# Kernel optimization log

Measured on AMD Instinct MI355X. Metric: run time of the kernel, lower is better.

Reference implementation:

```python
import jax, jax.numpy as jnp
import numpy as np

H = 1024      # hidden_size
NH = 16       # num_attention_heads
DH = H // NH  # head_dim
EPS_LN = 1e-5


def _ln(x, g, b):
    m = x.mean(-1, keepdims=True)
    v = ((x - m) ** 2).mean(-1, keepdims=True)
    return (x - m) * jax.lax.rsqrt(v + EPS_LN) * g + b


def _gelu(x):
    return jax.nn.gelu(x, approximate=False)


def _split_heads(x, B, S):
    return x.reshape(B, S, NH, DH).transpose(0, 2, 1, 3)  # [B,NH,S,DH]


def setup_inputs() -> dict:
    key = jax.random.key(0)
    ks = jax.random.split(key, 16)
    std = 0.02
    d = {
        'hidden_states': jax.random.normal(ks[0], (4, 1024, H), jnp.float32),
        'wq': jax.random.normal(ks[1], (H, H), jnp.float32) * std,
        'wk': jax.random.normal(ks[2], (H, H), jnp.float32) * std,
        'wv': jax.random.normal(ks[3], (H, H), jnp.float32) * std,
        'wo': jax.random.normal(ks[4], (H, H), jnp.float32) * std,
        'mha_in_w': jax.random.normal(ks[5], (3 * H, H), jnp.float32) * std,   # nn.MultiheadAttention in_proj (no bias)
        'mha_out_w': jax.random.normal(ks[6], (H, H), jnp.float32) * std,
        'wt': jax.random.normal(ks[7], (NH, H), jnp.float32) * std,            # W_t
        'ttm_ln_g': jnp.ones((NH,), jnp.float32),
        'ttm_ln_b': jnp.zeros((NH,), jnp.float32),
        'thp_w': jax.random.normal(ks[8], (H, NH), jnp.float32) * std,         # temp_hidden_proj Linear(NH->H)
        'thp_b': jnp.zeros((H,), jnp.float32),
        'thp_ln_g': jnp.ones((H,), jnp.float32),
        'thp_ln_b': jnp.zeros((H,), jnp.float32),
        'tn_w1': jax.random.normal(ks[9], (H, 2 * H), jnp.float32) * std,      # temp_net Linear(2H->H)
        'tn_b1': jnp.zeros((H,), jnp.float32),
        'tn_ln_g': jnp.ones((H,), jnp.float32),
        'tn_ln_b': jnp.zeros((H,), jnp.float32),
        'tn_w2': jax.random.normal(ks[10], (1, H), jnp.float32) * std,         # temp_net Linear(H->1)
        'tn_b2': jnp.zeros((1,), jnp.float32),
    }
    return d


def reference(hidden_states, wq, wk, wv, wo, mha_in_w, mha_out_w, wt,
              ttm_ln_g, ttm_ln_b, thp_w, thp_b, thp_ln_g, thp_ln_b,
              tn_w1, tn_b1, tn_ln_g, tn_ln_b, tn_w2, tn_b2):
    x = hidden_states
    B, S, _ = x.shape
    scale = DH ** -0.5

    # ---- compute_ttm: T(x) = sigmoid(LN(W_t @ MHA(x,x,x))) (eval mode, step<100 branch) ----
    qkv = jnp.einsum('bsh,oh->bso', x, mha_in_w)  # [B,S,3H]
    mq, mk, mv = jnp.split(qkv, 3, axis=-1)
    mq, mk, mv = (_split_heads(t, B, S) for t in (mq, mk, mv))
    mprob = jax.nn.softmax(jnp.einsum('bhqd,bhkd->bhqk', mq, mk) * scale, axis=-1)
    mctx = jnp.einsum('bhqk,bhkd->bhqd', mprob, mv).transpose(0, 2, 1, 3).reshape(B, S, H)
    ttm_out = jnp.einsum('bsh,oh->bso', mctx, mha_out_w)
    temp = jax.nn.sigmoid(_ln(jnp.einsum('bsh,nh->bsn', ttm_out, wt), ttm_ln_g, ttm_ln_b))
    T0 = 1.0 + 0.1 * (temp - 0.5)  # [B,S,NH]

    # ---- compute_gsot ----
    T_base = jax.nn.sigmoid(_gelu(_ln(jnp.einsum('bsn,hn->bsh', T0, thp_w) + thp_b, thp_ln_g, thp_ln_b)))  # [B,S,H]
    temps = [T_base[:, :, 0:1]]
    for _ in range(2):
        comb = jnp.concatenate([x, T_base], axis=-1)  # [B,S,2H]
        h = _gelu(_ln(jnp.einsum('bsc,hc->bsh', comb, tn_w1) + tn_b1, tn_ln_g, tn_ln_b))
        Ti = jax.nn.sigmoid(jax.nn.sigmoid(jnp.einsum('bsh,oh->bso', h, tn_w2) + tn_b2))  # double sigmoid, [B,S,1]
        temps.append(Ti)
        T_base = jnp.broadcast_to(Ti, (B, S, H))
    scale_temps = jnp.stack(temps, axis=1)  # [B,3,S,1]

    # ---- temperature weights: normalized over the broadcast [B,NH,S,S] tensor ----
    tw = scale_temps.mean(axis=1)  # [B,S,1]
    Nt = B * NH * S * S            # expanded element count (torch .std() is unbiased over it)
    mu = tw.mean()
    var_b = ((tw - mu) ** 2).mean()
    std_u = jnp.sqrt(var_b * (Nt / (Nt - 1)))
    eps = jnp.finfo(tw.dtype).eps
    twn = 1.0 + (tw - mu) / (std_u + eps)  # [B,S,1], per-query scalar

    # ---- main attention ----
    q = _split_heads(jnp.einsum('bsh,oh->bso', x, wq), B, S)
    k = _split_heads(jnp.einsum('bsh,oh->bso', x, wk), B, S)
    v = _split_heads(jnp.einsum('bsh,oh->bso', x, wv), B, S)
    scores = jnp.einsum('bhqd,bhkd->bhqk', q, k) * scale
    scores = scores * twn[:, None, :, :]  # broadcast over heads and keys
    probs = jax.nn.softmax(scores, axis=-1)
    ctx = jnp.einsum('bhqk,bhkd->bhqd', probs, v).transpose(0, 2, 1, 3).reshape(B, S, H)
    context = jnp.einsum('bsh,oh->bso', ctx, wo)
    return (context, scale_temps)
```

## Files before the change

### kernel.cpp

```cpp
#include <hip/hip_runtime.h>
#include <hip/hip_bf16.h>

#define DEV __device__ __forceinline__

typedef short bf16x8 __attribute__((ext_vector_type(8)));
typedef short bf16x4 __attribute__((ext_vector_type(4)));
typedef float f32x4 __attribute__((ext_vector_type(4)));

static constexpr int B_  = 4;
static constexpr int S_  = 1024;
static constexpr int H_  = 1024;
static constexpr int NH_ = 16;
static constexpr int DH_ = 64;
static constexpr int BS_ = B_ * S_;
static constexpr int H6_ = 6 * H_;

DEV void gld16(const void* g, void* l) {
  __builtin_amdgcn_global_load_lds(
      (__attribute__((address_space(1))) void*)(unsigned long long)g,
      (__attribute__((address_space(3))) void*)(unsigned)(unsigned long long)l,
      16, 0, 0);
}

DEV f32x4 pv_mfma(bf16x4 a, bf16x4 b, f32x4 c) {
#if __has_builtin(__builtin_amdgcn_mfma_f32_16x16x16bf16_1k)
  return __builtin_amdgcn_mfma_f32_16x16x16bf16_1k(a, b, c, 0, 0, 0);
#else
  asm volatile("v_mfma_f32_16x16x16_bf16 %0, %1, %2, %0" : "+v"(c) : "v"(a), "v"(b));
  return c;
#endif
}

DEV float wred_sum(float v) {
#pragma unroll
  for (int o = 32; o; o >>= 1) v += __shfl_xor(v, o);
  return v;
}
DEV float bred_sum(float v, float* sh) {
  v = wred_sum(v);
  const int tid = threadIdx.x;
  if ((tid & 63) == 0) sh[tid >> 6] = v;
  __syncthreads();
  v = sh[0] + sh[1] + sh[2] + sh[3];
  __syncthreads();
  return v;
}
DEV float geluf(float x) { return 0.5f * x * (1.f + erff(x * 0.70710678118654752f)); }

struct CastSeg { const float* src; unsigned short* dst; int n; };
struct PrepArgs {
  CastSeg s[7];
  const float* wt; const float* wout; float* weff;
  const float* w1; float* rsum;
};
__global__ __launch_bounds__(256) void prep_k(PrepArgs a) {
  const int y = blockIdx.y, tid = threadIdx.x;
  if (y < 7) {
    const CastSeg g = a.s[y];
    int i = (blockIdx.x * 256 + tid) * 4;
    if (i >= g.n) return;
    float4 v = *(const float4*)(g.src + i);
    __hip_bfloat16 o0 = __float2bfloat16(v.x), o1 = __float2bfloat16(v.y);
    __hip_bfloat16 o2 = __float2bfloat16(v.z), o3 = __float2bfloat16(v.w);
    ushort4 o;
    o.x = *(unsigned short*)&o0; o.y = *(unsigned short*)&o1;
    o.z = *(unsigned short*)&o2; o.w = *(unsigned short*)&o3;
    *(ushort4*)(g.dst + i) = o;
  } else if (y == 7) {
    if (blockIdx.x >= 256) return;
    const int h = (blockIdx.x & 15) * 64 + (tid & 63), ng = tid >> 6;
    const int o0 = (blockIdx.x >> 4) * 64;
    float acc[4] = {0.f, 0.f, 0.f, 0.f};
#pragma unroll 8
    for (int o = o0; o < o0 + 64; o++) {
      float wv = a.wout[(size_t)o * H_ + h];
#pragma unroll
      for (int i = 0; i < 4; i++) acc[i] += a.wt[(size_t)(ng * 4 + i) * H_ + o] * wv;
    }
#pragma unroll
    for (int i = 0; i < 4; i++) atomicAdd(&a.weff[(size_t)(ng * 4 + i) * H_ + h], acc[i]);
  } else {
    if (blockIdx.x >= 256) return;
    const int row = blockIdx.x * 4 + (tid >> 6), lane = tid & 63;
    float s = 0.f;
#pragma unroll
    for (int j = 0; j < 16; j++) s += a.w1[(size_t)row * 2048 + 1024 + lane + j * 64];
    s = wred_sum(s);
    if (lane == 0) a.rsum[row] = s;
  }
}

__global__ __launch_bounds__(256) void gemm_qkv_k(
    const __hip_bfloat16* __restrict__ Ap, const __hip_bfloat16* __restrict__ Wp,
    __hip_bfloat16* __restrict__ Cp, __hip_bfloat16* __restrict__ vt2) {
  constexpr int BK = 32;
  __shared__ __align__(16) short smem[8448];
  short* sA = smem;
  short* sB = smem + 4096;
  short* sT = smem;
  const int tid = threadIdx.x;
  const int wave = tid >> 6, lane = tid & 63;
  const int wm = wave >> 1, wn = wave & 1;
  const int lr = lane & 15, kq = lane >> 4;
  const int bx = blockIdx.x, by = blockIdx.y;
  const short* Ab = (const short*)Ap + (long long)by * 128 * H_;
  const short* Wb = (const short*)Wp + (long long)bx * 128 * H_;

  f32x4 acc[4][4];
#pragma unroll
  for (int i = 0; i < 4; i++)
#pragma unroll
    for (int j = 0; j < 4; j++) acc[i][j] = f32x4{0.f, 0.f, 0.f, 0.f};

  for (int k0 = 0; k0 < H_; k0 += BK) {
#pragma unroll
    for (int r = 0; r < 2; r++) {
      int idx = r * 256 + tid;
      gld16(Ab + (long long)(idx >> 2) * H_ + k0 + (idx & 3) * 8, sA + (size_t)idx * 8);
    }
#pragma unroll
    for (int r = 0; r < 2; r++) {
      int idx = r * 256 + tid;
      gld16(Wb + (long long)(idx >> 2) * H_ + k0 + (idx & 3) * 8, sB + (size_t)idx * 8);
    }
    __syncthreads();
    bf16x8 af[4], bfr[4];
#pragma unroll
    for (int i = 0; i < 4; i++)
      af[i] = *(const bf16x8*)(sA + (wm * 64 + i * 16 + lr) * BK + kq * 8);
#pragma unroll
    for (int j = 0; j < 4; j++)
      bfr[j] = *(const bf16x8*)(sB + (wn * 64 + j * 16 + lr) * BK + kq * 8);
#pragma unroll
    for (int i = 0; i < 4; i++)
#pragma unroll
      for (int j = 0; j < 4; j++)
        acc[i][j] = __builtin_amdgcn_mfma_f32_16x16x32_bf16(af[i], bfr[j], acc[i][j], 0, 0, 0);
    __syncthreads();
  }

  const bool isV = (bx >= 16 && bx < 24) || (bx >= 40);
  if (!isV) {
    const long long row0 = (long long)by * 128 + wm * 64 + kq * 4;
    const long long col0 = (long long)bx * 128 + wn * 64 + lr;
#pragma unroll
    for (int i = 0; i < 4; i++)
#pragma unroll
      for (int j = 0; j < 4; j++)
#pragma unroll
        for (int r = 0; r < 4; r++)
          Cp[(row0 + i * 16 + r) * H6_ + col0 + j * 16] = __float2bfloat16(acc[i][j][r]);
  } else {
    const int sel = bx >= 40;
    const int h0 = (bx - (sel ? 40 : 16)) * 2;
    const int b = by >> 3, s0 = (by & 7) * 128;
#pragma unroll
    for (int hh = 0; hh < 2; hh++) {
      __syncthreads();
      if (wn == hh) {
#pragma unroll
        for (int i = 0; i < 4; i++)
#pragma unroll
          for (int j = 0; j < 4; j++)
#pragma unroll
            for (int r = 0; r < 4; r++) {
              __hip_bfloat16 v = __float2bfloat16(acc[i][j][r]);
              sT[(j * 16 + lr) * 132 + wm * 64 + i * 16 + kq * 4 + r] = *(short*)&v;
            }
      }
      __syncthreads();
      const int bh2 = sel * 64 + b * 16 + h0 + hh;
      short* dst = (short*)vt2 + (size_t)bh2 * DH_ * S_ + s0;
#pragma unroll
      for (int c = 0; c < 8; c++) {
        int flat = c * 256 + tid;
        int d = flat >> 5, s4 = (flat & 31) * 4;
        *(short4*)(dst + (size_t)d * S_ + s4) = *(short4*)(sT + d * 132 + s4);
      }
    }
  }
}

template <int MT, int NT, int WR, int WC, bool MID>
__global__ __launch_bounds__(256) void gemm_bt(
    const __hip_bfloat16* __restrict__ Ap, const __hip_bfloat16* __restrict__ Wp,
    float* __restrict__ Cp, int K, int lda, int ldw, int ldc,
    const __hip_bfloat16* __restrict__ Ap2, float* __restrict__ Cmid, int kmid) {
  constexpr int BM = WR * MT * 16;
  constexpr int BN = WC * NT * 16;
  constexpr int BK = 32;
  __shared__ __align__(16) short sA[BM * BK];
  __shared__ __align__(16) short sB[BN * BK];
  const int tid = threadIdx.x;
  const int wave = tid >> 6, lane = tid & 63;
  const int wm = wave / WC, wn = wave % WC;
  const int lr = lane & 15, kq = lane >> 4;
  const short* Ab = (const short*)Ap + (long long)blockIdx.y * BM * lda;
  const short* Ab2 = MID ? (const short*)Ap2 + (long long)blockIdx.y * BM * lda : nullptr;
  const short* Wb = (const short*)Wp + (long long)blockIdx.x * BN * ldw;
  const long long row0 = (long long)blockIdx.y * BM + wm * MT * 16 + kq * 4;
  const long long col0 = (long long)blockIdx.x * BN + wn * NT * 16 + lr;

  f32x4 acc[MT][NT];
#pragma unroll
  for (int i = 0; i < MT; i++)
#pragma unroll
    for (int j = 0; j < NT; j++) acc[i][j] = f32x4{0.f, 0.f, 0.f, 0.f};

  for (int k0 = 0; k0 < K; k0 += BK) {
    const short* Asrc;
    int ka;
    if (MID && k0 >= kmid) { Asrc = Ab2; ka = k0 - kmid; }
    else { Asrc = Ab; ka = k0; }
#pragma unroll
    for (int r = 0; r < BM / 64; r++) {
      int idx = r * 256 + tid;
      gld16(Asrc + (long long)(idx >> 2) * lda + ka + (idx & 3) * 8, sA + (size_t)idx * 8);
    }
#pragma unroll
    for (int r = 0; r < BN / 64; r++) {
      int idx = r * 256 + tid;
      gld16(Wb + (long long)(idx >> 2) * ldw + k0 + (idx & 3) * 8, sB + (size_t)idx * 8);
    }
    __syncthreads();
    bf16x8 af[MT], bfr[NT];
#pragma unroll
    for (int i = 0; i < MT; i++)
      af[i] = *(const bf16x8*)(sA + (wm * MT * 16 + i * 16 + lr) * BK + kq * 8);
#pragma unroll
    for (int j = 0; j < NT; j++)
      bfr[j] = *(const bf16x8*)(sB + (wn * NT * 16 + j * 16 + lr) * BK + kq * 8);
#pragma unroll
    for (int i = 0; i < MT; i++)
#pragma unroll
      for (int j = 0; j < NT; j++)
        acc[i][j] = __builtin_amdgcn_mfma_f32_16x16x32_bf16(af[i], bfr[j], acc[i][j], 0, 0, 0);
    if constexpr (MID) {
      if (k0 + BK == kmid) {
#pragma unroll
        for (int i = 0; i < MT; i++)
#pragma unroll
          for (int j = 0; j < NT; j++)
#pragma unroll
            for (int r = 0; r < 4; r++)
              Cmid[(row0 + i * 16 + r) * ldc + col0 + j * 16] = acc[i][j][r];
      }
    }
    __syncthreads();
  }
#pragma unroll
  for (int i = 0; i < MT; i++)
#pragma unroll
    for (int j = 0; j < NT; j++)
#pragma unroll
      for (int r = 0; r < 4; r++)
        Cp[(row0 + i * 16 + r) * ldc + col0 + j * 16] = acc[i][j][r];
}

template <bool TTM>
__global__ __launch_bounds__(256) void flash_k(
    const __hip_bfloat16* __restrict__ qkvB,
    const __hip_bfloat16* __restrict__ vt,
    const float* __restrict__ twn,
    __hip_bfloat16* __restrict__ ctx,
    float scale, int ldq) {
  __shared__ __align__(16) short sK[2][128 * 64];
  __shared__ __align__(16) short sVT[2][64 * 128];
  const int bh = blockIdx.x, b = bh >> 4, h = bh & 15;
  const int qb = blockIdx.y;
  const int tid = threadIdx.x, lane = tid & 63, wid = tid >> 6;
  const int lr = lane & 15, quad = lane >> 4;
  const short* qg = (const short*)qkvB + ((size_t)(b * S_) + qb * 128) * ldq + h * 64;
  const short* kg = (const short*)qkvB + (size_t)b * S_ * ldq + H_ + h * 64;
  const short* vg = (const short*)vt + (size_t)bh * DH_ * S_;

  auto stage = [&](int kt, int buf) {
#pragma unroll
    for (int i = 0; i < 4; i++) {
      int idx = i * 256 + tid;
      int row = idx >> 3, cp = idx & 7;
      int c = cp ^ (row & 7);
      gld16(kg + (size_t)(kt * 128 + row) * ldq + c * 8, &sK[buf][(size_t)idx * 8]);
    }
#pragma unroll
    for (int i = 0; i < 4; i++) {
      int idx = i * 256 + tid;
      int row = idx >> 4, cp = idx & 15;
      int c = cp ^ (row & 15);
      gld16(vg + (size_t)row * S_ + kt * 128 + c * 8, &sVT[buf][(size_t)idx * 8]);
    }
  };

  bf16x8 bq[2][2];
#pragma unroll
  for (int nt = 0; nt < 2; nt++)
#pragma unroll
    for (int kk = 0; kk < 2; kk++)
      bq[nt][kk] =
          *(const bf16x8*)(qg + (size_t)(wid * 32 + nt * 16 + lr) * ldq + kk * 32 + quad * 8);

  float fs[2];
#pragma unroll
  for (int nt = 0; nt < 2; nt++) {
    int q = qb * 128 + wid * 32 + nt * 16 + lr;
    fs[nt] = TTM ? scale : scale * twn[b * S_ + q];
  }
  f32x4 O[2][4];
#pragma unroll
  for (int nt = 0; nt < 2; nt++)
#pragma unroll
    for (int dt = 0; dt < 4; dt++) O[nt][dt] = f32x4{0.f, 0.f, 0.f, 0.f};
  float lrow[2] = {0.f, 0.f};

  stage(0, 0);
  __syncthreads();

  for (int kt = 0; kt < 8; kt++) {
    const int cur = kt & 1;
    if (kt < 7) stage(kt + 1, cur ^ 1);
    const short* sKc = sK[cur];
    const short* sVc = sVT[cur];

    f32x4 Sa[8][2];
#pragma unroll
    for (int mt = 0; mt < 8; mt++)
#pragma unroll
      for (int nt = 0; nt < 2; nt++) Sa[mt][nt] = f32x4{0.f, 0.f, 0.f, 0.f};
#pragma unroll
    for (int mt = 0; mt < 8; mt++)
#pragma unroll
      for (int kk = 0; kk < 2; kk++) {
        int row = mt * 16 + lr;
        int cp = (kk * 4 + quad) ^ (lr & 7);
        bf16x8 ak = *(const bf16x8*)(sKc + row * 64 + cp * 8);
#pragma unroll
        for (int nt = 0; nt < 2; nt++)
          Sa[mt][nt] = __builtin_amdgcn_mfma_f32_16x16x32_bf16(ak, bq[nt][kk], Sa[mt][nt], 0, 0, 0);
      }

    bf16x4 Pf[8][2];
#pragma unroll
    for (int nt = 0; nt < 2; nt++) {
      float ls = 0.f;
#pragma unroll
      for (int mt = 0; mt < 8; mt++) {
        float p0 = __expf(Sa[mt][nt][0] * fs[nt]);
        float p1 = __expf(Sa[mt][nt][1] * fs[nt]);
        float p2 = __expf(Sa[mt][nt][2] * fs[nt]);
        float p3 = __expf(Sa[mt][nt][3] * fs[nt]);
        ls += (p0 + p1) + (p2 + p3);
        __hip_bfloat16 h0 = __float2bfloat16(p0), h1 = __float2bfloat16(p1);
        __hip_bfloat16 h2 = __float2bfloat16(p2), h3 = __float2bfloat16(p3);
        bf16x4 pk;
        pk[0] = *(short*)&h0; pk[1] = *(short*)&h1;
        pk[2] = *(short*)&h2; pk[3] = *(short*)&h3;
        Pf[mt][nt] = pk;
      }
      ls += __shfl_xor(ls, 16);
      ls += __shfl_xor(ls, 32);
      lrow[nt] += ls;
    }

#pragma unroll
    for (int mt = 0; mt < 8; mt++)
#pragma unroll
      for (int dt = 0; dt < 4; dt++) {
        int row = dt * 16 + lr;
        int cp = (2 * mt + (quad >> 1)) ^ lr;
        bf16x4 bv = *(const bf16x4*)(sVc + row * 128 + cp * 8 + (quad & 1) * 4);
#pragma unroll
        for (int nt = 0; nt < 2; nt++) O[nt][dt] = pv_mfma(Pf[mt][nt], bv, O[nt][dt]);
      }

    __syncthreads();
  }

#pragma unroll
  for (int nt = 0; nt < 2; nt++)
#pragma unroll
    for (int r = 0; r < 4; r++) {
      float li = __shfl(lrow[nt], quad * 4 + r);
      float inv = 1.f / li;
      int q = qb * 128 + wid * 32 + nt * 16 + quad * 4 + r;
      __hip_bfloat16* op = ctx + ((size_t)(b * S_) + q) * H_ + h * 64 + lr;
#pragma unroll
      for (int dt = 0; dt < 4; dt++)
        op[dt * 16] = __float2bfloat16(O[nt][dt][r] * inv);
    }
}

__global__ __launch_bounds__(256) void wtproj_k(const __hip_bfloat16* __restrict__ mctx,
                                                const float* __restrict__ weff,
                                                const float* __restrict__ g,
                                                const float* __restrict__ be,
                                                float* __restrict__ T0) {
  __shared__ float sC[4][256];
  const int tid = threadIdx.x, lane = tid & 63, wid = tid >> 6;
  const int lr = lane & 15, quad = lane >> 4;
  const int bs0 = blockIdx.x * 16;
  const short* aG = (const short*)mctx + (size_t)(bs0 + lr) * H_ + wid * 256;
  const float* bG = weff + (size_t)lr * H_ + wid * 256;
  f32x4 acc = f32x4{0.f, 0.f, 0.f, 0.f};
#pragma unroll
  for (int it = 0; it < 8; it++) {
    bf16x8 a = *(const bf16x8*)(aG + it * 32 + quad * 8);
    float4 b0 = *(const float4*)(bG + it * 32 + quad * 8);
    float4 b1 = *(const float4*)(bG + it * 32 + quad * 8 + 4);
    bf16x8 bb;
#pragma unroll
    for (int j = 0; j < 4; j++) {
      __hip_bfloat16 c0 = __float2bfloat16((&b0.x)[j]);
      __hip_bfloat16 c1 = __float2bfloat16((&b1.x)[j]);
      bb[j] = *(short*)&c0;
      bb[4 + j] = *(short*)&c1;
    }
    acc = __builtin_amdgcn_mfma_f32_16x16x32_bf16(a, bb, acc, 0, 0, 0);
  }
#pragma unroll
  for (int r = 0; r < 4; r++) sC[wid][(quad * 4 + r) * 16 + lr] = acc[r];
  __syncthreads();
  float tot = sC[0][tid] + sC[1][tid] + sC[2][tid] + sC[3][tid];
  const int n = tid & 15;
  float mean = tot;
#pragma unroll
  for (int o = 1; o < 16; o <<= 1) mean += __shfl_xor(mean, o);
  mean *= (1.f / 16.f);
  float d = tot - mean;
  float var = d * d;
#pragma unroll
  for (int o = 1; o < 16; o <<= 1) var += __shfl_xor(var, o);
  var *= (1.f / 16.f);
  float z = d * rsqrtf(var + 1e-5f) * g[n] + be[n];
  float t = 1.f / (1.f + expf(-z));
  T0[(size_t)blockIdx.x * 256 + tid] = 1.f + 0.1f * (t - 0.5f);
}

__global__ __launch_bounds__(256) void thp_k(const float* __restrict__ T0,
                                             const float* __restrict__ w,
                                             const float* __restrict__ bb,
                                             const float* __restrict__ g,
                                             const float* __restrict__ be,
                                             __hip_bfloat16* __restrict__ Tb,
                                             float* __restrict__ t0out) {
  __shared__ float sh[4];
  __shared__ float t0s[16];
  const int bs = blockIdx.x, tid = threadIdx.x;
  if (tid < 16) t0s[tid] = T0[(size_t)bs * 16 + tid];
  __syncthreads();
  float y[4];
#pragma unroll
  for (int i = 0; i < 4; i++) {
    int hh = tid + i * 256;
    const float* wr = w + (size_t)hh * 16;
    float a = bb[hh];
#pragma unroll
    for (int n = 0; n < 16; n++) a += t0s[n] * wr[n];
    y[i] = a;
  }
  float mean = bred_sum(y[0] + y[1] + y[2] + y[3], sh) * (1.f / 1024.f);
  float q = 0.f;
#pragma unroll
  for (int i = 0; i < 4; i++) { float d = y[i] - mean; q += d * d; }
  float var = bred_sum(q, sh) * (1.f / 1024.f);
  const float rs = rsqrtf(var + 1e-5f);
#pragma unroll
  for (int i = 0; i < 4; i++) {
    int hh = tid + i * 256;
    float z = (y[i] - mean) * rs * g[hh] + be[hh];
    float t = 1.f / (1.f + expf(-geluf(z)));
    Tb[(size_t)bs * H_ + hh] = __float2bfloat16(t);
    if (hh == 0) t0out[bs] = t;
  }
}

__global__ __launch_bounds__(256) void hlnrd2_k(const float* __restrict__ xw1a,
                                                const float* __restrict__ tbwf,
                                                const float* __restrict__ rsum,
                                                const float* __restrict__ b1,
                                                const float* __restrict__ g,
                                                const float* __restrict__ be,
                                                const float* __restrict__ w2,
                                                const float* __restrict__ b2,
                                                float* __restrict__ t1out,
                                                float* __restrict__ t2out) {
  __shared__ float sh[4];
  const int bs = blockIdx.x, tid = threadIdx.x;
  float xa[4], bv[4], y[4];
#pragma unroll
  for (int i = 0; i < 4; i++) {
    int hh = tid + i * 256;
    xa[i] = xw1a[(size_t)bs * H_ + hh];
    bv[i] = b1[hh];
    y[i] = tbwf[(size_t)bs * H_ + hh] + bv[i];
  }
  float T1, T2;
#pragma unroll
  for (int iter = 0; iter < 2; iter++) {
    float mean = bred_sum(y[0] + y[1] + y[2] + y[3], sh) * (1.f / 1024.f);
    float q = 0.f;
#pragma unroll
    for (int i = 0; i < 4; i++) { float d = y[i] - mean; q += d * d; }
    float var = bred_sum(q, sh) * (1.f / 1024.f);
    const float rs = rsqrtf(var + 1e-5f);
    float s = 0.f;
#pragma unroll
    for (int i = 0; i < 4; i++) {
      int hh = tid + i * 256;
      float z = (y[i] - mean) * rs * g[hh] + be[hh];
      s += geluf(z) * w2[hh];
    }
    s = bred_sum(s, sh);
    float d = s + b2[0];
    float t = 1.f / (1.f + expf(-d));
    t = 1.f / (1.f + expf(-t));
    if (iter == 0) {
      T1 = t;
#pragma unroll
      for (int i = 0; i < 4; i++) {
        int hh = tid + i * 256;
        y[i] = xa[i] + T1 * rsum[hh] + bv[i];
      }
    } else {
      T2 = t;
    }
  }
  if (tid == 0) { t1out[bs] = T1; t2out[bs] = T2; }
}

__global__ __launch_bounds__(256) void stats_k(const float* __restrict__ t0,
                                               const float* __restrict__ t1,
                                               const float* __restrict__ t2,
                                               float* __restrict__ twn,
                                               float* __restrict__ out2) {
  __shared__ float sh[4];
  const int tid = threadIdx.x;
  float s = 0.f;
  for (int i = tid; i < BS_; i += 256) s += (t0[i] + t1[i] + t2[i]) * (1.f / 3.f);
  const float mu = bred_sum(s, sh) * (1.f / (float)BS_);
  float q = 0.f;
  for (int i = tid; i < BS_; i += 256) {
    float tw = (t0[i] + t1[i] + t2[i]) * (1.f / 3.f);
    float d = tw - mu;
    q += d * d;
  }
  const float var = bred_sum(q, sh) * (1.f / (float)BS_);
  const float stdu = sqrtf(var);
  const float inv = 1.f / (stdu + 1.1920929e-07f);
  for (int i = tid; i < BS_; i += 256) {
    float tw = (t0[i] + t1[i] + t2[i]) * (1.f / 3.f);
    twn[i] = 1.f + (tw - mu) * inv;
  }
  for (int i = tid; i < 3 * BS_; i += 256) {
    int b = i / 3072, r = i - b * 3072;
    int j = r >> 10, ss = r & 1023;
    const float* tp = (j == 0) ? t0 : ((j == 1) ? t1 : t2);
    out2[i] = tp[b * S_ + ss];
  }
}

extern "C" void kernel_launch(void* const* d_in, const int* in_sizes, int n_in,
                              void* d_out, int out_size, void* d_ws, size_t ws_size,
                              hipStream_t stream) {
  (void)in_sizes; (void)n_in; (void)out_size; (void)ws_size;
  const float* x     = (const float*)d_in[0];
  const float* wq    = (const float*)d_in[1];
  const float* wk    = (const float*)d_in[2];
  const float* wv    = (const float*)d_in[3];
  const float* wo    = (const float*)d_in[4];
  const float* w_in  = (const float*)d_in[5];
  const float* w_out = (const float*)d_in[6];
  const float* wt    = (const float*)d_in[7];
  const float* ttm_g = (const float*)d_in[8];
  const float* ttm_b = (const float*)d_in[9];
  const float* thp_w = (const float*)d_in[10];
  const float* thp_b = (const float*)d_in[11];
  const float* thp_g = (const float*)d_in[12];
  const float* thp_e = (const float*)d_in[13];
  const float* w1    = (const float*)d_in[14];
  const float* b1    = (const float*)d_in[15];
  const float* tn_g  = (const float*)d_in[16];
  const float* tn_e  = (const float*)d_in[17];
  const float* w2    = (const float*)d_in[18];
  const float* b2    = (const float*)d_in[19];

  char* ws = (char*)d_ws;
  size_t off = 0;
  auto alloc = [&](size_t bytes) {
    void* p = ws + off;
    off = (off + bytes + 255) & ~(size_t)255;
    return p;
  };

  __hip_bfloat16* xb    = (__hip_bfloat16*)alloc((size_t)BS_ * H_ * 2);
  __hip_bfloat16* wcat  = (__hip_bfloat16*)alloc((size_t)H6_ * H_ * 2);
  __hip_bfloat16* wob   = (__hip_bfloat16*)alloc((size_t)H_ * H_ * 2);
  __hip_bfloat16* w1b   = (__hip_bfloat16*)alloc((size_t)H_ * 2 * H_ * 2);
  __hip_bfloat16* qkv2  = (__hip_bfloat16*)alloc((size_t)BS_ * H6_ * 2);
  __hip_bfloat16* vt2   = (__hip_bfloat16*)alloc((size_t)128 * DH_ * S_ * 2);
  __hip_bfloat16* mctxb = (__hip_bfloat16*)alloc((size_t)BS_ * H_ * 2);
  __hip_bfloat16* tob   = (__hip_bfloat16*)alloc((size_t)BS_ * H_ * 2);
  float* weff  = (float*)alloc((size_t)NH_ * H_ * 4);
  float* T0    = (float*)alloc((size_t)BS_ * NH_ * 4);
  float* xw1a  = (float*)alloc((size_t)BS_ * H_ * 4);
  float* tbw   = (float*)alloc((size_t)BS_ * H_ * 4);
  float* temps = (float*)alloc((size_t)3 * BS_ * 4);
  float* twn   = (float*)alloc((size_t)BS_ * 4);
  float* rsum  = (float*)alloc((size_t)H_ * 4);

  const float scale = 0.125f;
  dim3 blk(256);

  hipMemsetAsync(weff, 0, (size_t)NH_ * H_ * 4, stream);
  PrepArgs pa;
  pa.s[0] = {x, (unsigned short*)xb, BS_ * H_};
  pa.s[1] = {w_in, (unsigned short*)wcat, 3 * H_ * H_};
  pa.s[2] = {wq, (unsigned short*)wcat + (size_t)3 * H_ * H_, H_ * H_};
  pa.s[3] = {wk, (unsigned short*)wcat + (size_t)4 * H_ * H_, H_ * H_};
  pa.s[4] = {wv, (unsigned short*)wcat + (size_t)5 * H_ * H_, H_ * H_};
  pa.s[5] = {wo, (unsigned short*)wob, H_ * H_};
  pa.s[6] = {w1, (unsigned short*)w1b, 2 * H_ * H_};
  pa.wt = wt; pa.wout = w_out; pa.weff = weff; pa.w1 = w1; pa.rsum = rsum;
  prep_k<<<dim3((BS_ * H_ + 1023) / 1024, 9), blk, 0, stream>>>(pa);

  gemm_qkv_k<<<dim3(H6_ / 128, BS_ / 128), blk, 0, stream>>>(xb, wcat, qkv2, vt2);

  flash_k<true><<<dim3(64, 8), blk, 0, stream>>>(qkv2, vt2, (const float*)nullptr, mctxb,
                                                 scale, H6_);
  wtproj_k<<<BS_ / 16, blk, 0, stream>>>(mctxb, weff, ttm_g, ttm_b, T0);
  thp_k<<<BS_, blk, 0, stream>>>(T0, thp_w, thp_b, thp_g, thp_e, tob, temps);

  gemm_bt<4, 2, 2, 2, true><<<dim3(H_ / 64, BS_ / 128), blk, 0, stream>>>(
      xb, w1b, tbw, 2 * H_, H_, 2 * H_, H_, tob, xw1a, H_);
  hlnrd2_k<<<BS_, blk, 0, stream>>>(xw1a, tbw, rsum, b1, tn_g, tn_e, w2, b2,
                                    temps + BS_, temps + 2 * BS_);
  stats_k<<<1, blk, 0, stream>>>(temps, temps + BS_, temps + 2 * BS_, twn,
                                 (float*)d_out + (size_t)BS_ * H_);

  flash_k<false><<<dim3(64, 8), blk, 0, stream>>>(qkv2 + 3 * H_,
                                                  vt2 + (size_t)64 * DH_ * S_, twn, mctxb,
                                                  scale, H6_);
  gemm_bt<4, 2, 2, 2, false><<<dim3(H_ / 64, BS_ / 128), blk, 0, stream>>>(
      mctxb, wob, (float*)d_out, H_, H_, H_, H_, nullptr, nullptr, 0);
}
```

Before: 401.9 us.

## Double-buffer LDS tiles in QKV and generic bf16 GEMM kernels

Both the fused QKV GEMM and the templated gemm_bt now allocate two LDS stages and issue global-to-LDS loads for the next K tile before computing on the current one. This overlaps memory latency with MFMA work instead of waiting on each tile's load. It doubles the LDS footprint per block, which may lower occupancy. Correctness relies on the existing end-of-iteration barrier to protect buffer reuse.

```diff
diff --git a/kernel.cpp b/kernel.cpp
--- a/kernel.cpp
+++ b/kernel.cpp
@@ -94,10 +94,7 @@
     const __hip_bfloat16* __restrict__ Ap, const __hip_bfloat16* __restrict__ Wp,
     __hip_bfloat16* __restrict__ Cp, __hip_bfloat16* __restrict__ vt2) {
   constexpr int BK = 32;
-  __shared__ __align__(16) short smem[8448];
-  short* sA = smem;
-  short* sB = smem + 4096;
-  short* sT = smem;
+  __shared__ __align__(16) short smem[16384];
   const int tid = threadIdx.x;
   const int wave = tid >> 6, lane = tid & 63;
   const int wm = wave >> 1, wn = wave & 1;
@@ -106,13 +103,9 @@
   const short* Ab = (const short*)Ap + (long long)by * 128 * H_;
   const short* Wb = (const short*)Wp + (long long)bx * 128 * H_;
 
-  f32x4 acc[4][4];
-#pragma unroll
-  for (int i = 0; i < 4; i++)
-#pragma unroll
-    for (int j = 0; j < 4; j++) acc[i][j] = f32x4{0.f, 0.f, 0.f, 0.f};
-
-  for (int k0 = 0; k0 < H_; k0 += BK) {
+  auto stage = [&](int k0, int buf) {
+    short* sA = smem + buf * 4096;
+    short* sB = smem + 8192 + buf * 4096;
 #pragma unroll
     for (int r = 0; r < 2; r++) {
       int idx = r * 256 + tid;
@@ -123,7 +116,22 @@
       int idx = r * 256 + tid;
       gld16(Wb + (long long)(idx >> 2) * H_ + k0 + (idx & 3) * 8, sB + (size_t)idx * 8);
     }
-    __syncthreads();
+  };
+
+  f32x4 acc[4][4];
+#pragma unroll
+  for (int i = 0; i < 4; i++)
+#pragma unroll
+    for (int j = 0; j < 4; j++) acc[i][j] = f32x4{0.f, 0.f, 0.f, 0.f};
+
+  stage(0, 0);
+  __syncthreads();
+
+  for (int it = 0; it < H_ / BK; it++) {
+    const int cur = it & 1;
+    if (it < H_ / BK - 1) stage((it + 1) * BK, cur ^ 1);
+    const short* sA = smem + cur * 4096;
+    const short* sB = smem + 8192 + cur * 4096;
     bf16x8 af[4], bfr[4];
 #pragma unroll
     for (int i = 0; i < 4; i++)
@@ -151,6 +159,7 @@
         for (int r = 0; r < 4; r++)
           Cp[(row0 + i * 16 + r) * H6_ + col0 + j * 16] = __float2bfloat16(acc[i][j][r]);
   } else {
+    short* sT = smem;
     const int sel = bx >= 40;
     const int h0 = (bx - (sel ? 40 : 16)) * 2;
     const int b = by >> 3, s0 = (by & 7) * 128;
@@ -189,8 +198,8 @@
   constexpr int BM = WR * MT * 16;
   constexpr int BN = WC * NT * 16;
   constexpr int BK = 32;
-  __shared__ __align__(16) short sA[BM * BK];
-  __shared__ __align__(16) short sB[BN * BK];
+  __shared__ __align__(16) short sAs[2][BM * BK];
+  __shared__ __align__(16) short sBs[2][BN * BK];
   const int tid = threadIdx.x;
   const int wave = tid >> 6, lane = tid & 63;
   const int wm = wave / WC, wn = wave % WC;
@@ -201,13 +210,7 @@
   const long long row0 = (long long)blockIdx.y * BM + wm * MT * 16 + kq * 4;
   const long long col0 = (long long)blockIdx.x * BN + wn * NT * 16 + lr;
 
-  f32x4 acc[MT][NT];
-#pragma unroll
-  for (int i = 0; i < MT; i++)
-#pragma unroll
-    for (int j = 0; j < NT; j++) acc[i][j] = f32x4{0.f, 0.f, 0.f, 0.f};
-
-  for (int k0 = 0; k0 < K; k0 += BK) {
+  auto stage = [&](int k0, int buf) {
     const short* Asrc;
     int ka;
     if (MID && k0 >= kmid) { Asrc = Ab2; ka = k0 - kmid; }
@@ -215,14 +218,29 @@
 #pragma unroll
     for (int r = 0; r < BM / 64; r++) {
       int idx = r * 256 + tid;
-      gld16(Asrc + (long long)(idx >> 2) * lda + ka + (idx & 3) * 8, sA + (size_t)idx * 8);
+      gld16(Asrc + (long long)(idx >> 2) * lda + ka + (idx & 3) * 8, &sAs[buf][(size_t)idx * 8]);
     }
 #pragma unroll
     for (int r = 0; r < BN / 64; r++) {
       int idx = r * 256 + tid;
-      gld16(Wb + (long long)(idx >> 2) * ldw + k0 + (idx & 3) * 8, sB + (size_t)idx * 8);
-    }
-    __syncthreads();
+      gld16(Wb + (long long)(idx >> 2) * ldw + k0 + (idx & 3) * 8, &sBs[buf][(size_t)idx * 8]);
+    }
+  };
+
+  f32x4 acc[MT][NT];
+#pragma unroll
+  for (int i = 0; i < MT; i++)
+#pragma unroll
+    for (int j = 0; j < NT; j++) acc[i][j] = f32x4{0.f, 0.f, 0.f, 0.f};
+
+  stage(0, 0);
+  __syncthreads();
+
+  for (int k0 = 0; k0 < K; k0 += BK) {
+    const int cur = (k0 / BK) & 1;
+    if (k0 + BK < K) stage(k0 + BK, cur ^ 1);
+    const short* sA = sAs[cur];
+    const short* sB = sBs[cur];
     bf16x8 af[MT], bfr[NT];
 #pragma unroll
     for (int i = 0; i < MT; i++)
@@ -610,7 +628,7 @@
   const float scale = 0.125f;
   dim3 blk(256);
 
-  hipMemsetAsync(weff, 0, (size_t)NH_ * H_ * 4, stream);
+  (void)hipMemsetAsync(weff, 0, (size_t)NH_ * H_ * 4, stream);
   PrepArgs pa;
   pa.s[0] = {x, (unsigned short*)xb, BS_ * H_};
   pa.s[1] = {w_in, (unsigned short*)wcat, 3 * H_ * H_};
```

New measurement: 400.5 us. No clear change (-0.3%).
